# Kernel optimization log

Hardware: AMD Instinct MI355X
Metric: run time of the kernel (lower is better)

## Reference

```python
import jax, jax.numpy as jnp
import numpy as np

N, E = 50000, 400000
F_IN, HID, OUT, H = 128, 64, 40, 4
SLOPE = 0.2


def setup_inputs() -> dict:
    key = jax.random.key(0)
    ks = jax.random.split(key, 20)

    def gn(k, shape, scale=0.05):
        return jax.random.normal(k, shape, dtype=jnp.float32) * scale

    inp = {
        "node_inputs": jax.random.normal(ks[0], (N, F_IN), dtype=jnp.float32),
        "src": jax.random.randint(ks[1], (E,), 0, N),
        "dst": jax.random.randint(ks[2], (E,), 0, N),
    }
    # (in_dim, per-head out_dim) per layer; residual linear only when in != heads*out
    dims = [(F_IN, HID), (H * HID, HID), (H * HID, OUT)]
    i = 3
    for l, (fin, d) in enumerate(dims):
        inp[f"w_src{l}"] = gn(ks[i], (fin, H * d)); i += 1
        inp[f"b_src{l}"] = jnp.zeros((H * d,), jnp.float32)
        inp[f"w_dst{l}"] = gn(ks[i], (fin, H * d)); i += 1
        inp[f"b_dst{l}"] = jnp.zeros((H * d,), jnp.float32)
        inp[f"attn{l}"] = gn(ks[i], (H, d)); i += 1
        if fin != H * d:
            inp[f"w_res{l}"] = gn(ks[i], (fin, H * d)); i += 1
            inp[f"b_res{l}"] = jnp.zeros((H * d,), jnp.float32)
    return inp


def _gatv2_layer(x, src, dst, w_s, b_s, w_d, b_d, attn, res):
    # x: [N, F]; res: [N, H*D] residual term (already projected or identity)
    n = x.shape[0]
    h, d = attn.shape
    hs = (x @ w_s + b_s).reshape(n, h, d)   # feat_src
    hd = (x @ w_d + b_d).reshape(n, h, d)   # feat_dst
    e = hs[src] + hd[dst]                    # [E, H, D]
    e = jnp.where(e > 0, e, SLOPE * e)       # LeakyReLU
    logits = jnp.einsum('ehd,hd->eh', e, attn)  # [E, H]
    # edge softmax over incoming edges of each dst node
    m = jax.ops.segment_max(logits, dst, num_segments=n)
    z = jnp.exp(logits - m[dst])
    s = jax.ops.segment_sum(z, dst, num_segments=n)
    a = z / s[dst]                            # [E, H]
    out = jax.ops.segment_sum(hs[src] * a[:, :, None], dst, num_segments=n)  # [N, H, D]
    return out + res.reshape(n, h, d)


def reference(node_inputs, src, dst,
              w_src0, b_src0, w_dst0, b_dst0, attn0, w_res0, b_res0,
              w_src1, b_src1, w_dst1, b_dst1, attn1,
              w_src2, b_src2, w_dst2, b_dst2, attn2, w_res2, b_res2):
    x = node_inputs
    # layer 0: in=128 != heads*hid -> linear residual
    x = _gatv2_layer(x, src, dst, w_src0, b_src0, w_dst0, b_dst0, attn0,
                     x @ w_res0 + b_res0)
    x = x.reshape(x.shape[0], -1)  # flatten heads
    # layer 1: in == heads*hid -> identity residual
    x = _gatv2_layer(x, src, dst, w_src1, b_src1, w_dst1, b_dst1, attn1, x)
    x = x.reshape(x.shape[0], -1)
    # layer 2: in=256 != heads*out -> linear residual
    x = _gatv2_layer(x, src, dst, w_src2, b_src2, w_dst2, b_dst2, attn2,
                     x @ w_res2 + b_res2)
    # mean over heads: [N, H, OUT] -> [N, OUT]
    return x.mean(axis=-2)
```

## Files before the change

kernel.cpp:

```cpp
#include <hip/hip_runtime.h>
#include <hip/hip_bf16.h>
#include <math.h>

#define SLOPE 0.2f

typedef unsigned short bf16_t;
typedef short bh8 __attribute__((ext_vector_type(8)));
typedef float f32x4 __attribute__((ext_vector_type(4)));

__device__ __forceinline__ float bf2f(bf16_t x) {
    return __uint_as_float((unsigned)x << 16);
}
__device__ __forceinline__ bf16_t f2bf(float v) {
    unsigned u = __float_as_uint(v);
    return (bf16_t)((u + 0x7FFFu + ((u >> 16) & 1u)) >> 16);
}
__device__ __forceinline__ ushort2 pk_f2bf(float a, float b) {
    __hip_bfloat162 h2 = __float22bfloat162_rn(float2{a, b});
    union { __hip_bfloat162 h; ushort2 u; } u;
    u.h = h2;
    return u.u;
}


__global__ void hist_dst(const int* __restrict__ dst, int E, int* __restrict__ deg) {
    int e = blockIdx.x * 256 + threadIdx.x;
    if (e < E) atomicAdd(&deg[dst[e]], 1);
}

__global__ void deg_chunk_sum(const int* __restrict__ deg, int n, int* __restrict__ chunk_sums) {
    __shared__ int sm[256];
    int base = blockIdx.x * 1024;
    int s = 0;
    for (int i = threadIdx.x; i < 1024; i += 256) {
        int idx = base + i;
        if (idx < n) s += deg[idx];
    }
    sm[threadIdx.x] = s;
    __syncthreads();
    for (int off = 128; off > 0; off >>= 1) {
        if (threadIdx.x < off) sm[threadIdx.x] += sm[threadIdx.x + off];
        __syncthreads();
    }
    if (threadIdx.x == 0) chunk_sums[blockIdx.x] = sm[0];
}

__global__ void scan_chunk_sums(int* __restrict__ chunk_sums, int nchunks) {
    __shared__ int sm[256];
    int t = threadIdx.x;
    if (t < nchunks) sm[t] = chunk_sums[t];
    __syncthreads();
    if (t == 0) {
        int run = 0;
        for (int i = 0; i < nchunks; i++) { int v = sm[i]; sm[i] = run; run += v; }
    }
    __syncthreads();
    if (t < nchunks) chunk_sums[t] = sm[t];
}

__global__ void scan_write(const int* __restrict__ deg, int n,
                           const int* __restrict__ chunk_sums,
                           int* __restrict__ row_start, int Etot) {
    int base = blockIdx.x * 1024;
    int t = threadIdx.x;
    int v[4];
    int tsum = 0;
#pragma unroll
    for (int j = 0; j < 4; j++) {
        int idx = base + t * 4 + j;
        v[j] = (idx < n) ? deg[idx] : 0;
        tsum += v[j];
    }
    __shared__ int sm[256];
    sm[t] = tsum;
    __syncthreads();
    for (int off = 1; off < 256; off <<= 1) {
        int x = (t >= off) ? sm[t - off] : 0;
        __syncthreads();
        sm[t] += x;
        __syncthreads();
    }
    int excl = sm[t] - tsum + chunk_sums[blockIdx.x];
#pragma unroll
    for (int j = 0; j < 4; j++) {
        int idx = base + t * 4 + j;
        if (idx < n) row_start[idx] = excl;
        excl += v[j];
    }
    if (blockIdx.x == 0 && t == 0) row_start[n] = Etot;
}

__global__ void scatter_edges(const int* __restrict__ dst, const int* __restrict__ src, int E,
                              const int* __restrict__ row_start,
                              int* __restrict__ fill, int* __restrict__ src_sorted) {
    int e = blockIdx.x * 256 + threadIdx.x;
    if (e < E) {
        int d_ = dst[e];
        int pos = row_start[d_] + atomicAdd(&fill[d_], 1);
        src_sorted[pos] = src[e];
    }
}


__global__ void convert_weights(
    const float* __restrict__ w0, const float* __restrict__ w1, const float* __restrict__ w2,
    const float* __restrict__ w3, const float* __restrict__ w4,
    const float* __restrict__ w5, const float* __restrict__ w6,
    const float* __restrict__ wr2, const float* __restrict__ br2,
    bf16_t* __restrict__ t0, bf16_t* __restrict__ t1, bf16_t* __restrict__ t2,
    bf16_t* __restrict__ t3, bf16_t* __restrict__ t4,
    bf16_t* __restrict__ t5, bf16_t* __restrict__ t6,
    bf16_t* __restrict__ teff, float* __restrict__ b_eff)
{
    int b = blockIdx.x, t = threadIdx.x;
    const float* W; bf16_t* T; int K, Nc, lb;
    if (b < 384) {
        int g = b / 128; lb = b - g * 128;
        W = g == 0 ? w0 : (g == 1 ? w1 : w2);
        T = g == 0 ? t0 : (g == 1 ? t1 : t2);
        K = 128; Nc = 256;
    } else if (b < 896) {
        int g = (b - 384) / 256; lb = (b - 384) - g * 256;
        W = g == 0 ? w3 : w4; T = g == 0 ? t3 : t4;
        K = 256; Nc = 256;
    } else if (b < 1280) {
        int g = (b - 896) / 192; lb = (b - 896) - g * 192;
        W = g == 0 ? w5 : w6; T = g == 0 ? t5 : t6;
        K = 256; Nc = 160;
    } else {
        lb = b - 1280;
        int idx = lb * 256 + t;
        int n = idx >> 8, k = idx & 255;
        float v = 0.f;
        if (n < 40)
            v = 0.25f * (wr2[(size_t)k * 160 + n] + wr2[(size_t)k * 160 + 40 + n] +
                         wr2[(size_t)k * 160 + 80 + n] + wr2[(size_t)k * 160 + 120 + n]);
        teff[idx] = f2bf(v);
        if (lb == 0 && t < 40)
            b_eff[t] = 0.25f * (br2[t] + br2[40 + t] + br2[80 + t] + br2[120 + t]);
        return;
    }
    int idx = lb * 256 + t;
    int n = idx / K, k = idx - n * K;
    float v = (n < Nc) ? W[(size_t)k * Nc + n] : 0.f;
    T[idx] = f2bf(v);
}


template <typename TA, int NOUT, int KTOT, int NPAD, bool SPLIT40, bool HAS_EFF>
__global__ __launch_bounds__(256) void gemm_lds(
    const TA* __restrict__ A,
    const bf16_t* __restrict__ Wt0, const bf16_t* __restrict__ Wt1, const bf16_t* __restrict__ Wt2,
    const float* __restrict__ bias0, const float* __restrict__ bias1, const float* __restrict__ bias2,
    bf16_t* __restrict__ C0, bf16_t* __restrict__ C1, bf16_t* __restrict__ C2,
    const bf16_t* __restrict__ Wte, const float* __restrict__ biase, float* __restrict__ Ce,
    int M, int Nc)
{
    constexpr int LSTR = KTOT + 8;
    constexpr int ESTR = 38;
    __shared__ bf16_t As[64 * LSTR];
    __shared__ bf16_t Ep[4 * 64 * ESTR];

    int tid = threadIdx.x;
    int lane = tid & 63, w = tid >> 6;
    int lm = lane & 15, lq = lane >> 4;
    int m0 = blockIdx.x * 64;

    const bf16_t* Wts[3] = {Wt0, Wt1, Wt2};
    const float* biases[3] = {bias0, bias1, bias2};
    bf16_t* Cs[3] = {C0, C1, C2};

    if (sizeof(TA) == 4) {
#pragma unroll
        for (int it = 0; it < 4; it++) {
            int idx = tid + it * 256;
            int r = idx >> 4, c = idx & 15;
            int gm = m0 + r; if (gm >= M) gm = M - 1;
            const float* ap = (const float*)A + (size_t)gm * KTOT + c * 8;
            float4 lo = *(const float4*)ap;
            float4 hi = *(const float4*)(ap + 4);
            ushort2 p0 = pk_f2bf(lo.x, lo.y), p1 = pk_f2bf(lo.z, lo.w);
            ushort2 p2 = pk_f2bf(hi.x, hi.y), p3 = pk_f2bf(hi.z, hi.w);
            bh8 v = { (short)p0.x, (short)p0.y, (short)p1.x, (short)p1.y,
                      (short)p2.x, (short)p2.y, (short)p3.x, (short)p3.y };
            *(bh8*)(As + r * LSTR + c * 8) = v;
        }
    } else {
#pragma unroll
        for (int it = 0; it < 8; it++) {
            int idx = tid + it * 256;
            int r = idx >> 5, c = idx & 31;
            int gm = m0 + r; if (gm >= M) gm = M - 1;
            bh8 v = *(const bh8*)((const bf16_t*)A + (size_t)gm * KTOT + c * 8);
            *(bh8*)(As + r * LSTR + c * 8) = v;
        }
    }
    __syncthreads();

    bf16_t* ep = Ep + w * (64 * ESTR);
    constexpr int NCHUNK = (NPAD + 127) / 128;

#pragma unroll
    for (int chunk = 0; chunk < NCHUNK; chunk++) {
        int n0 = chunk * 128 + w * 32;
        if (n0 >= NPAD) continue;

        int boff[NOUT][2];
#pragma unroll
        for (int o = 0; o < NOUT; o++)
#pragma unroll
            for (int nt = 0; nt < 2; nt++)
                boff[o][nt] = (n0 + nt * 16 + lm) * KTOT + lq * 8;

        f32x4 acc[NOUT][4][2];
#pragma unroll
        for (int o = 0; o < NOUT; o++)
#pragma unroll
            for (int i = 0; i < 4; i++)
#pragma unroll
                for (int j = 0; j < 2; j++)
                    acc[o][i][j] = (f32x4){0.f, 0.f, 0.f, 0.f};

#pragma unroll
        for (int kc = 0; kc < KTOT / 32; kc++) {
            bh8 af[4];
#pragma unroll
            for (int mt = 0; mt < 4; mt++)
                af[mt] = *(const bh8*)(As + (mt * 16 + lm) * LSTR + kc * 32 + lq * 8);
#pragma unroll
            for (int o = 0; o < NOUT; o++) {
                bh8 bf[2];
#pragma unroll
                for (int nt = 0; nt < 2; nt++)
                    bf[nt] = *(const bh8*)(Wts[o] + boff[o][nt] + kc * 32);
#pragma unroll
                for (int mt = 0; mt < 4; mt++)
#pragma unroll
                    for (int nt = 0; nt < 2; nt++)
                        acc[o][mt][nt] = __builtin_amdgcn_mfma_f32_16x16x32_bf16(af[mt], bf[nt], acc[o][mt][nt], 0, 0, 0);
            }
        }

#pragma unroll
        for (int o = 0; o < NOUT; o++) {
#pragma unroll
            for (int nt = 0; nt < 2; nt++) {
                int gn = n0 + nt * 16 + lm;
                float bv = (gn < Nc) ? biases[o][gn] : 0.f;
#pragma unroll
                for (int mt = 0; mt < 4; mt++)
#pragma unroll
                    for (int r = 0; r < 4; r++)
                        ep[(mt * 16 + lq * 4 + r) * ESTR + nt * 16 + lm] = f2bf(acc[o][mt][nt][r] + bv);
            }
#pragma unroll
            for (int it = 0; it < 4; it++) {
                int row = it * 16 + (lane >> 2);
                int cc = (lane & 3) * 8;
                bh8 v = *(const bh8*)(ep + row * ESTR + cc);
                int gm = m0 + row;
                int cg = n0 + cc;
                if (gm < M && cg < Nc) {
                    size_t cb = SPLIT40 ? (size_t)(cg + 24 * (cg / 40)) : (size_t)cg;
                    size_t rs = SPLIT40 ? 256 : (size_t)Nc;
                    *(bh8*)(Cs[o] + (size_t)gm * rs + cb) = v;
                }
            }
        }
    }

    if (HAS_EFF && w < 2) {
        int beoff[2];
#pragma unroll
        for (int nt = 0; nt < 2; nt++)
            beoff[nt] = (w * 32 + nt * 16 + lm) * KTOT + lq * 8;
        f32x4 acc_e[4][2];
#pragma unroll
        for (int i = 0; i < 4; i++)
#pragma unroll
            for (int j = 0; j < 2; j++)
                acc_e[i][j] = (f32x4){0.f, 0.f, 0.f, 0.f};
#pragma unroll
        for (int kc = 0; kc < KTOT / 32; kc++) {
            bh8 af[4];
#pragma unroll
            for (int mt = 0; mt < 4; mt++)
                af[mt] = *(const bh8*)(As + (mt * 16 + lm) * LSTR + kc * 32 + lq * 8);
            bh8 be[2];
#pragma unroll
            for (int nt = 0; nt < 2; nt++)
                be[nt] = *(const bh8*)(Wte + beoff[nt] + kc * 32);
#pragma unroll
            for (int mt = 0; mt < 4; mt++)
#pragma unroll
                for (int nt = 0; nt < 2; nt++)
                    acc_e[mt][nt] = __builtin_amdgcn_mfma_f32_16x16x32_bf16(af[mt], be[nt], acc_e[mt][nt], 0, 0, 0);
        }
#pragma unroll
        for (int nt = 0; nt < 2; nt++) {
            int gn = w * 32 + nt * 16 + lm;
            if (gn >= 40) continue;
            float bv = biase[gn];
#pragma unroll
            for (int mt = 0; mt < 4; mt++)
#pragma unroll
                for (int r = 0; r < 4; r++) {
                    int gm = m0 + mt * 16 + lq * 4 + r;
                    if (gm < M) Ce[(size_t)gm * 40 + gn] = acc_e[mt][nt][r] + bv;
                }
        }
    }
}


__device__ __forceinline__ float edge_logit(const float h[4], const float hdf[4], const float at[4]) {
    float p = 0.f;
#pragma unroll
    for (int j = 0; j < 4; j++) {
        float q = h[j] + hdf[j];
        float lr = fmaxf(q, SLOPE * q);
        p += lr * at[j];
    }
    p += __shfl_xor(p, 1, 64);
    p += __shfl_xor(p, 2, 64);
    p += __shfl_xor(p, 4, 64);
    p += __shfl_xor(p, 8, 64);
    return p;
}

__device__ __forceinline__ void chain_update(float logit, const float h[4],
                                             float& m, float& l, float* a) {
    if (logit > m) {
        float sc = __expf(m - logit);
        l = l * sc + 1.f;
#pragma unroll
        for (int j = 0; j < 4; j++) a[j] = a[j] * sc + h[j];
        m = logit;
    } else {
        float p = __expf(logit - m);
        l += p;
#pragma unroll
        for (int j = 0; j < 4; j++) a[j] += p * h[j];
    }
}

template <int DVALID, bool FINAL, bool RES_INPLACE>
__global__ __launch_bounds__(256) void gat_agg_wave(
    const bf16_t* __restrict__ hs, const bf16_t* __restrict__ hd,
    const float* __restrict__ attn,
    const int* __restrict__ row_start, const int* __restrict__ src_sorted,
    bf16_t* __restrict__ P, float* __restrict__ out_final, int N)
{
    int w = threadIdx.x >> 6, l = threadIdx.x & 63;
    int n = blockIdx.x * 4 + w;
    if (n >= N) return;
    int h = l >> 4;
    int f0 = 4 * l;
    int dp = 4 * (l & 15);

    float at[4];
#pragma unroll
    for (int j = 0; j < 4; j++)
        at[j] = (dp + j < DVALID) ? attn[h * DVALID + dp + j] : 0.f;
    ushort4 hv = *(const ushort4*)(hd + (unsigned)(n * 256 + f0));
    float hdf[4] = { bf2f(hv.x), bf2f(hv.y), bf2f(hv.z), bf2f(hv.w) };

    int s = row_start[n], e = row_start[n + 1];

    float cm[4] = {-INFINITY, -INFINITY, -INFINITY, -INFINITY};
    float cl[4] = {0.f, 0.f, 0.f, 0.f};
    float ca[4][4] = {};

    int i = s;
    for (; i + 4 <= e; i += 4) {
        int sn0 = src_sorted[i], sn1 = src_sorted[i + 1];
        int sn2 = src_sorted[i + 2], sn3 = src_sorted[i + 3];
        ushort4 r0 = *(const ushort4*)(hs + (unsigned)(sn0 * 256 + f0));
        ushort4 r1 = *(const ushort4*)(hs + (unsigned)(sn1 * 256 + f0));
        ushort4 r2 = *(const ushort4*)(hs + (unsigned)(sn2 * 256 + f0));
        ushort4 r3 = *(const ushort4*)(hs + (unsigned)(sn3 * 256 + f0));
        float h0[4] = { bf2f(r0.x), bf2f(r0.y), bf2f(r0.z), bf2f(r0.w) };
        float h1[4] = { bf2f(r1.x), bf2f(r1.y), bf2f(r1.z), bf2f(r1.w) };
        float h2[4] = { bf2f(r2.x), bf2f(r2.y), bf2f(r2.z), bf2f(r2.w) };
        float h3[4] = { bf2f(r3.x), bf2f(r3.y), bf2f(r3.z), bf2f(r3.w) };
        float p0 = edge_logit(h0, hdf, at);
        float p1 = edge_logit(h1, hdf, at);
        float p2 = edge_logit(h2, hdf, at);
        float p3 = edge_logit(h3, hdf, at);
        chain_update(p0, h0, cm[0], cl[0], ca[0]);
        chain_update(p1, h1, cm[1], cl[1], ca[1]);
        chain_update(p2, h2, cm[2], cl[2], ca[2]);
        chain_update(p3, h3, cm[3], cl[3], ca[3]);
    }
    for (; i < e; i++) {
        int sn0 = src_sorted[i];
        ushort4 r0 = *(const ushort4*)(hs + (unsigned)(sn0 * 256 + f0));
        float h0[4] = { bf2f(r0.x), bf2f(r0.y), bf2f(r0.z), bf2f(r0.w) };
        float p0 = edge_logit(h0, hdf, at);
        chain_update(p0, h0, cm[0], cl[0], ca[0]);
    }

    float v[4] = {0.f, 0.f, 0.f, 0.f};
    if (e > s) {
        float M = fmaxf(fmaxf(cm[0], cm[1]), fmaxf(cm[2], cm[3]));
        float L = 0.f;
#pragma unroll
        for (int c = 0; c < 4; c++) {
            float sc = __expf(cm[c] - M);
            L += sc * cl[c];
#pragma unroll
            for (int j = 0; j < 4; j++) v[j] += sc * ca[c][j];
        }
        float inv = 1.f / L;
#pragma unroll
        for (int j = 0; j < 4; j++) v[j] *= inv;
    }

    if (FINAL) {
#pragma unroll
        for (int j = 0; j < 4; j++) {
            v[j] += __shfl_xor(v[j], 16, 64);
            v[j] += __shfl_xor(v[j], 32, 64);
        }
        if (l < DVALID / 4) {
            float4* op = (float4*)(out_final + (unsigned)(n * DVALID + 4 * l));
            float4 cur = *op;
            cur.x += 0.25f * v[0]; cur.y += 0.25f * v[1];
            cur.z += 0.25f * v[2]; cur.w += 0.25f * v[3];
            *op = cur;
        }
    } else {
        unsigned oi = (unsigned)(n * 256 + f0);
        if (RES_INPLACE) {
            ushort4 pv = *(const ushort4*)(P + oi);
            v[0] += bf2f(pv.x); v[1] += bf2f(pv.y);
            v[2] += bf2f(pv.z); v[3] += bf2f(pv.w);
        }
        ushort4 ov = { f2bf(v[0]), f2bf(v[1]), f2bf(v[2]), f2bf(v[3]) };
        *(ushort4*)(P + oi) = ov;
    }
}


extern "C" void kernel_launch(void* const* d_in, const int* in_sizes, int n_in,
                              void* d_out, int out_size, void* d_ws, size_t ws_size,
                              hipStream_t stream) {
    const float* x0    = (const float*)d_in[0];
    const int*   src   = (const int*)d_in[1];
    const int*   dst   = (const int*)d_in[2];
    const float* w_src0 = (const float*)d_in[3];  const float* b_src0 = (const float*)d_in[4];
    const float* w_dst0 = (const float*)d_in[5];  const float* b_dst0 = (const float*)d_in[6];
    const float* attn0  = (const float*)d_in[7];
    const float* w_res0 = (const float*)d_in[8];  const float* b_res0 = (const float*)d_in[9];
    const float* w_src1 = (const float*)d_in[10]; const float* b_src1 = (const float*)d_in[11];
    const float* w_dst1 = (const float*)d_in[12]; const float* b_dst1 = (const float*)d_in[13];
    const float* attn1  = (const float*)d_in[14];
    const float* w_src2 = (const float*)d_in[15]; const float* b_src2 = (const float*)d_in[16];
    const float* w_dst2 = (const float*)d_in[17]; const float* b_dst2 = (const float*)d_in[18];
    const float* attn2  = (const float*)d_in[19];
    const float* w_res2 = (const float*)d_in[20]; const float* b_res2 = (const float*)d_in[21];

    const int N = in_sizes[0] / 128;
    const int E = in_sizes[1];
    float* out = (float*)d_out;
    (void)n_in; (void)out_size; (void)ws_size;

    char* ws = (char*)d_ws;
    size_t off = 0;
    auto alloc = [&](size_t bytes) {
        void* q = ws + off;
        off = (off + bytes + 255) & ~(size_t)255;
        return q;
    };
    int* deg        = (int*)alloc((size_t)2 * N * 4);
    int* fill       = deg + N;
    int* row_start  = (int*)alloc((size_t)(N + 1) * 4);
    int* chunk_sums = (int*)alloc(256 * 4);
    int* src_sorted = (int*)alloc((size_t)E * 4);
    bf16_t* t_src0 = (bf16_t*)alloc(256 * 128 * 2);
    bf16_t* t_dst0 = (bf16_t*)alloc(256 * 128 * 2);
    bf16_t* t_res0 = (bf16_t*)alloc(256 * 128 * 2);
    bf16_t* t_src1 = (bf16_t*)alloc(256 * 256 * 2);
    bf16_t* t_dst1 = (bf16_t*)alloc(256 * 256 * 2);
    bf16_t* t_src2 = (bf16_t*)alloc(192 * 256 * 2);
    bf16_t* t_dst2 = (bf16_t*)alloc(192 * 256 * 2);
    bf16_t* t_eff  = (bf16_t*)alloc(64 * 256 * 2);
    float*  b_eff  = (float*)alloc(64 * 4);
    const size_t elems = (size_t)N * 256;
    bf16_t* P  = (bf16_t*)alloc(elems * 2);
    bf16_t* HS = (bf16_t*)alloc(elems * 2);
    bf16_t* HD = (bf16_t*)alloc(elems * 2);

    hipMemsetAsync(deg, 0, (size_t)2 * N * 4, stream);
    int eblocks = (E + 255) / 256;
    int nchunks = (N + 1023) / 1024;
    hipLaunchKernelGGL(hist_dst, dim3(eblocks), dim3(256), 0, stream, dst, E, deg);
    hipLaunchKernelGGL(convert_weights, dim3(1344), dim3(256), 0, stream,
                       w_src0, w_dst0, w_res0, w_src1, w_dst1, w_src2, w_dst2, w_res2, b_res2,
                       t_src0, t_dst0, t_res0, t_src1, t_dst1, t_src2, t_dst2, t_eff, b_eff);
    hipLaunchKernelGGL(deg_chunk_sum, dim3(nchunks), dim3(256), 0, stream, deg, N, chunk_sums);
    hipLaunchKernelGGL(scan_chunk_sums, dim3(1), dim3(256), 0, stream, chunk_sums, nchunks);
    hipLaunchKernelGGL(scan_write, dim3(nchunks), dim3(256), 0, stream, deg, N, chunk_sums, row_start, E);
    hipLaunchKernelGGL(scatter_edges, dim3(eblocks), dim3(256), 0, stream, dst, src, E, row_start, fill, src_sorted);

    dim3 blk(256);
    int mtiles = (N + 63) / 64;
    int ab = (N + 3) / 4;

    hipLaunchKernelGGL((gemm_lds<float, 3, 128, 256, false, false>), dim3(mtiles), blk, 0, stream,
                       x0, t_src0, t_dst0, t_res0, b_src0, b_dst0, b_res0,
                       HS, HD, P,
                       (const bf16_t*)nullptr, (const float*)nullptr, (float*)nullptr,
                       N, 256);
    hipLaunchKernelGGL((gat_agg_wave<64, false, true>), dim3(ab), blk, 0, stream,
                       HS, HD, attn0, row_start, src_sorted, P, (float*)nullptr, N);

    hipLaunchKernelGGL((gemm_lds<bf16_t, 2, 256, 256, false, false>), dim3(mtiles), blk, 0, stream,
                       P, t_src1, t_dst1, (const bf16_t*)nullptr, b_src1, b_dst1, (const float*)nullptr,
                       HS, HD, (bf16_t*)nullptr,
                       (const bf16_t*)nullptr, (const float*)nullptr, (float*)nullptr,
                       N, 256);
    hipLaunchKernelGGL((gat_agg_wave<64, false, true>), dim3(ab), blk, 0, stream,
                       HS, HD, attn1, row_start, src_sorted, P, (float*)nullptr, N);

    hipLaunchKernelGGL((gemm_lds<bf16_t, 2, 256, 192, true, true>), dim3(mtiles), blk, 0, stream,
                       P, t_src2, t_dst2, (const bf16_t*)nullptr, b_src2, b_dst2, (const float*)nullptr,
                       HS, HD, (bf16_t*)nullptr,
                       t_eff, b_eff, out,
                       N, 160);
    hipLaunchKernelGGL((gat_agg_wave<40, true, false>), dim3(ab), blk, 0, stream,
                       HS, HD, attn2, row_start, src_sorted, (bf16_t*)nullptr, out, N);
}
```

Baseline: 481.4 us.

## Process two destination nodes per wave with 8-wide bf16 gathers in aggregation

The edge-softmax aggregation kernel now maps each half-wave (32 lanes) to one destination node, with every lane owning 8 features instead of 4. Gathers become 16-byte vector loads, the per-head logit reduction needs one fewer shuffle, and the grid is halved. The cost is doubled per-lane accumulator registers, which may reduce occupancy, plus a reworked head-mean write path for the final layer.

```diff
diff --git a/kernel.cpp b/kernel.cpp
--- a/kernel.cpp
+++ b/kernel.cpp
@@ -6,6 +6,7 @@
 
 typedef unsigned short bf16_t;
 typedef short bh8 __attribute__((ext_vector_type(8)));
+typedef unsigned short us8 __attribute__((ext_vector_type(8)));
 typedef float f32x4 __attribute__((ext_vector_type(4)));
 
 __device__ __forceinline__ float bf2f(bf16_t x) {
@@ -313,94 +314,98 @@
 }
 
 
-__device__ __forceinline__ float edge_logit(const float h[4], const float hdf[4], const float at[4]) {
-    float p = 0.f;
-#pragma unroll
-    for (int j = 0; j < 4; j++) {
-        float q = h[j] + hdf[j];
-        float lr = fmaxf(q, SLOPE * q);
-        p += lr * at[j];
-    }
-    p += __shfl_xor(p, 1, 64);
-    p += __shfl_xor(p, 2, 64);
-    p += __shfl_xor(p, 4, 64);
-    p += __shfl_xor(p, 8, 64);
-    return p;
-}
-
-__device__ __forceinline__ void chain_update(float logit, const float h[4],
-                                             float& m, float& l, float* a) {
+__device__ __forceinline__ void chain_update8(float logit, const float h[8],
+                                              float& m, float& l, float* a) {
     if (logit > m) {
         float sc = __expf(m - logit);
         l = l * sc + 1.f;
 #pragma unroll
-        for (int j = 0; j < 4; j++) a[j] = a[j] * sc + h[j];
+        for (int j = 0; j < 8; j++) a[j] = a[j] * sc + h[j];
         m = logit;
     } else {
         float p = __expf(logit - m);
         l += p;
 #pragma unroll
-        for (int j = 0; j < 4; j++) a[j] += p * h[j];
-    }
+        for (int j = 0; j < 8; j++) a[j] += p * h[j];
+    }
+}
+
+__device__ __forceinline__ float edge_logit8(const float h[8], const float hdf[8], const float at[8]) {
+    float p = 0.f;
+#pragma unroll
+    for (int j = 0; j < 8; j++) {
+        float q = h[j] + hdf[j];
+        float lr = fmaxf(q, SLOPE * q);
+        p += lr * at[j];
+    }
+    p += __shfl_xor(p, 1, 64);
+    p += __shfl_xor(p, 2, 64);
+    p += __shfl_xor(p, 4, 64);
+    return p;
+}
+
+__device__ __forceinline__ void us8_to_f(const us8 v, float* h) {
+#pragma unroll
+    for (int j = 0; j < 8; j++) h[j] = bf2f(v[j]);
 }
 
 template <int DVALID, bool FINAL, bool RES_INPLACE>
-__global__ __launch_bounds__(256) void gat_agg_wave(
+__global__ __launch_bounds__(256) void gat_agg_half(
     const bf16_t* __restrict__ hs, const bf16_t* __restrict__ hd,
     const float* __restrict__ attn,
     const int* __restrict__ row_start, const int* __restrict__ src_sorted,
     bf16_t* __restrict__ P, float* __restrict__ out_final, int N)
 {
-    int w = threadIdx.x >> 6, l = threadIdx.x & 63;
-    int n = blockIdx.x * 4 + w;
+    int w = threadIdx.x >> 6, lane = threadIdx.x & 63;
+    int half = lane >> 5, hl = lane & 31;
+    int n = blockIdx.x * 8 + w * 2 + half;
     if (n >= N) return;
-    int h = l >> 4;
-    int f0 = 4 * l;
-    int dp = 4 * (l & 15);
-
-    float at[4];
-#pragma unroll
-    for (int j = 0; j < 4; j++)
+    int f0 = hl * 8;
+    int h = hl >> 3;
+    int dp = (hl & 7) * 8;
+
+    float at[8], hdf[8];
+#pragma unroll
+    for (int j = 0; j < 8; j++)
         at[j] = (dp + j < DVALID) ? attn[h * DVALID + dp + j] : 0.f;
-    ushort4 hv = *(const ushort4*)(hd + (unsigned)(n * 256 + f0));
-    float hdf[4] = { bf2f(hv.x), bf2f(hv.y), bf2f(hv.z), bf2f(hv.w) };
+    us8 hv = *(const us8*)(hd + (unsigned)(n * 256 + f0));
+    us8_to_f(hv, hdf);
 
     int s = row_start[n], e = row_start[n + 1];
 
     float cm[4] = {-INFINITY, -INFINITY, -INFINITY, -INFINITY};
     float cl[4] = {0.f, 0.f, 0.f, 0.f};
-    float ca[4][4] = {};
+    float ca[4][8] = {};
 
     int i = s;
     for (; i + 4 <= e; i += 4) {
         int sn0 = src_sorted[i], sn1 = src_sorted[i + 1];
         int sn2 = src_sorted[i + 2], sn3 = src_sorted[i + 3];
-        ushort4 r0 = *(const ushort4*)(hs + (unsigned)(sn0 * 256 + f0));
-        ushort4 r1 = *(const ushort4*)(hs + (unsigned)(sn1 * 256 + f0));
-        ushort4 r2 = *(const ushort4*)(hs + (unsigned)(sn2 * 256 + f0));
-        ushort4 r3 = *(const ushort4*)(hs + (unsigned)(sn3 * 256 + f0));
-        float h0[4] = { bf2f(r0.x), bf2f(r0.y), bf2f(r0.z), bf2f(r0.w) };
-        float h1[4] = { bf2f(r1.x), bf2f(r1.y), bf2f(r1.z), bf2f(r1.w) };
-        float h2[4] = { bf2f(r2.x), bf2f(r2.y), bf2f(r2.z), bf2f(r2.w) };
-        float h3[4] = { bf2f(r3.x), bf2f(r3.y), bf2f(r3.z), bf2f(r3.w) };
-        float p0 = edge_logit(h0, hdf, at);
-        float p1 = edge_logit(h1, hdf, at);
-        float p2 = edge_logit(h2, hdf, at);
-        float p3 = edge_logit(h3, hdf, at);
-        chain_update(p0, h0, cm[0], cl[0], ca[0]);
-        chain_update(p1, h1, cm[1], cl[1], ca[1]);
-        chain_update(p2, h2, cm[2], cl[2], ca[2]);
-        chain_update(p3, h3, cm[3], cl[3], ca[3]);
+        us8 r0 = *(const us8*)(hs + (unsigned)(sn0 * 256 + f0));
+        us8 r1 = *(const us8*)(hs + (unsigned)(sn1 * 256 + f0));
+        us8 r2 = *(const us8*)(hs + (unsigned)(sn2 * 256 + f0));
+        us8 r3 = *(const us8*)(hs + (unsigned)(sn3 * 256 + f0));
+        float h0[8], h1[8], h2[8], h3[8];
+        us8_to_f(r0, h0); us8_to_f(r1, h1); us8_to_f(r2, h2); us8_to_f(r3, h3);
+        float p0 = edge_logit8(h0, hdf, at);
+        float p1 = edge_logit8(h1, hdf, at);
+        float p2 = edge_logit8(h2, hdf, at);
+        float p3 = edge_logit8(h3, hdf, at);
+        chain_update8(p0, h0, cm[0], cl[0], ca[0]);
+        chain_update8(p1, h1, cm[1], cl[1], ca[1]);
+        chain_update8(p2, h2, cm[2], cl[2], ca[2]);
+        chain_update8(p3, h3, cm[3], cl[3], ca[3]);
     }
     for (; i < e; i++) {
         int sn0 = src_sorted[i];
-        ushort4 r0 = *(const ushort4*)(hs + (unsigned)(sn0 * 256 + f0));
-        float h0[4] = { bf2f(r0.x), bf2f(r0.y), bf2f(r0.z), bf2f(r0.w) };
-        float p0 = edge_logit(h0, hdf, at);
-        chain_update(p0, h0, cm[0], cl[0], ca[0]);
-    }
-
-    float v[4] = {0.f, 0.f, 0.f, 0.f};
+        us8 r0 = *(const us8*)(hs + (unsigned)(sn0 * 256 + f0));
+        float h0[8];
+        us8_to_f(r0, h0);
+        float p0 = edge_logit8(h0, hdf, at);
+        chain_update8(p0, h0, cm[0], cl[0], ca[0]);
+    }
+
+    float v[8] = {};
     if (e > s) {
         float M = fmaxf(fmaxf(cm[0], cm[1]), fmaxf(cm[2], cm[3]));
         float L = 0.f;
@@ -409,35 +414,41 @@
             float sc = __expf(cm[c] - M);
             L += sc * cl[c];
 #pragma unroll
-            for (int j = 0; j < 4; j++) v[j] += sc * ca[c][j];
+            for (int j = 0; j < 8; j++) v[j] += sc * ca[c][j];
         }
         float inv = 1.f / L;
 #pragma unroll
-        for (int j = 0; j < 4; j++) v[j] *= inv;
+        for (int j = 0; j < 8; j++) v[j] *= inv;
     }
 
     if (FINAL) {
 #pragma unroll
-        for (int j = 0; j < 4; j++) {
+        for (int j = 0; j < 8; j++) {
+            v[j] += __shfl_xor(v[j], 8, 64);
             v[j] += __shfl_xor(v[j], 16, 64);
-            v[j] += __shfl_xor(v[j], 32, 64);
-        }
-        if (l < DVALID / 4) {
-            float4* op = (float4*)(out_final + (unsigned)(n * DVALID + 4 * l));
-            float4 cur = *op;
-            cur.x += 0.25f * v[0]; cur.y += 0.25f * v[1];
-            cur.z += 0.25f * v[2]; cur.w += 0.25f * v[3];
-            *op = cur;
+        }
+        if (hl < DVALID / 8 + 1 && h == 0 && dp < DVALID) {
+            float* op = out_final + (unsigned)(n * DVALID + dp);
+            float4 c0 = *(float4*)op;
+            float4 c1 = *(float4*)(op + 4);
+            c0.x += 0.25f * v[0]; c0.y += 0.25f * v[1];
+            c0.z += 0.25f * v[2]; c0.w += 0.25f * v[3];
+            c1.x += 0.25f * v[4]; c1.y += 0.25f * v[5];
+            c1.z += 0.25f * v[6]; c1.w += 0.25f * v[7];
+            *(float4*)op = c0;
+            *(float4*)(op + 4) = c1;
         }
     } else {
         unsigned oi = (unsigned)(n * 256 + f0);
         if (RES_INPLACE) {
-            ushort4 pv = *(const ushort4*)(P + oi);
-            v[0] += bf2f(pv.x); v[1] += bf2f(pv.y);
-            v[2] += bf2f(pv.z); v[3] += bf2f(pv.w);
-        }
-        ushort4 ov = { f2bf(v[0]), f2bf(v[1]), f2bf(v[2]), f2bf(v[3]) };
-        *(ushort4*)(P + oi) = ov;
+            us8 pv = *(const us8*)(P + oi);
+#pragma unroll
+            for (int j = 0; j < 8; j++) v[j] += bf2f(pv[j]);
+        }
+        us8 ov;
+#pragma unroll
+        for (int j = 0; j < 8; j++) ov[j] = f2bf(v[j]);
+        *(us8*)(P + oi) = ov;
     }
 }
 
@@ -505,14 +516,14 @@
 
     dim3 blk(256);
     int mtiles = (N + 63) / 64;
-    int ab = (N + 3) / 4;
+    int ab = (N + 7) / 8;
 
     hipLaunchKernelGGL((gemm_lds<float, 3, 128, 256, false, false>), dim3(mtiles), blk, 0, stream,
                        x0, t_src0, t_dst0, t_res0, b_src0, b_dst0, b_res0,
                        HS, HD, P,
                        (const bf16_t*)nullptr, (const float*)nullptr, (float*)nullptr,
                        N, 256);
-    hipLaunchKernelGGL((gat_agg_wave<64, false, true>), dim3(ab), blk, 0, stream,
+    hipLaunchKernelGGL((gat_agg_half<64, false, true>), dim3(ab), blk, 0, stream,
                        HS, HD, attn0, row_start, src_sorted, P, (float*)nullptr, N);
 
     hipLaunchKernelGGL((gemm_lds<bf16_t, 2, 256, 256, false, false>), dim3(mtiles), blk, 0, stream,
@@ -520,7 +531,7 @@
                        HS, HD, (bf16_t*)nullptr,
                        (const bf16_t*)nullptr, (const float*)nullptr, (float*)nullptr,
                        N, 256);
-    hipLaunchKernelGGL((gat_agg_wave<64, false, true>), dim3(ab), blk, 0, stream,
+    hipLaunchKernelGGL((gat_agg_half<64, false, true>), dim3(ab), blk, 0, stream,
                        HS, HD, attn1, row_start, src_sorted, P, (float*)nullptr, N);
 
     hipLaunchKernelGGL((gemm_lds<bf16_t, 2, 256, 192, true, true>), dim3(mtiles), blk, 0, stream,
@@ -528,6 +539,6 @@
                        HS, HD, (bf16_t*)nullptr,
                        t_eff, b_eff, out,
                        N, 160);
-    hipLaunchKernelGGL((gat_agg_wave<40, true, false>), dim3(ab), blk, 0, stream,
+    hipLaunchKernelGGL((gat_agg_half<40, true, false>), dim3(ab), blk, 0, stream,
                        HS, HD, attn2, row_start, src_sorted, (bf16_t*)nullptr, out, N);
 }
```

After: 455.2 us. -5.4%, faster.
